# Kernel optimization log

Hardware: AMD Instinct MI355X
Metric: run time of the kernel (lower is better)

## Reference

```python
import jax, jax.numpy as jnp
import numpy as np

B, T, D = 8, 4096, 128
NUM_CB, K = 8, 1024


def setup_inputs() -> dict:
    key = jax.random.key(0)
    k1, k2 = jax.random.split(key)
    embeddings = jax.random.normal(k1, (B, T, D), dtype=jnp.float32)
    # nn.init.uniform_(w, -1/codebook_size, 1/codebook_size)
    codebooks = jax.random.uniform(k2, (NUM_CB, K, D), dtype=jnp.float32,
                                   minval=-1.0 / K, maxval=1.0 / K)
    return {"embeddings": embeddings, "codebooks": codebooks}


def reference(embeddings, codebooks):
    """Residual VQ: returns (codes [B,T,C] int32, quantized [B,T,D], commitment_loss scalar)."""
    Bv, Tv, Dv = embeddings.shape
    flat = embeddings.reshape(-1, Dv)  # [N, D]

    def step(carry, cb_w):  # cb_w: [K, D]
        residual, quant, loss = carry
        # squared euclidean distance; argmin identical to torch.cdist argmin
        d2 = (jnp.sum(residual * residual, axis=-1, keepdims=True)
              - 2.0 * (residual @ cb_w.T)
              + jnp.sum(cb_w * cb_w, axis=-1))  # [N, K]
        idx = jnp.argmin(d2, axis=-1)  # [N]
        ql = cb_w[idx]  # [N, D] gather
        loss = loss + jnp.mean((jax.lax.stop_gradient(residual) - ql) ** 2)
        quant = quant + ql
        residual = residual - jax.lax.stop_gradient(ql)
        return (residual, quant, loss), idx

    init = (flat, jnp.zeros_like(flat), jnp.float32(0.0))
    (_, quant, loss), codes = jax.lax.scan(step, init, codebooks)
    codes = codes.T.reshape(Bv, Tv, codebooks.shape[0])  # [C,N] -> [B,T,C]
    quant = quant.reshape(Bv, Tv, Dv)
    # straight-through estimator
    quantized = embeddings + jax.lax.stop_gradient(quant - embeddings)
    return codes, quantized, loss / codebooks.shape[0]
```

## Files before the change

### kernel.cpp

```cpp
#include <hip/hip_runtime.h>


#define N_ROWS 32768
#define DIM    128
#define KCB    1024
#define NCB    8
#define MB     128
#define PC     256
#define NPASS  (KCB / PC)
#define LDA    132
#define LDB    68

__global__ __launch_bounds__(256) void zero_ws_kernel(double* lws) {
    if (threadIdx.x < NCB) lws[threadIdx.x] = 0.0;
}

__global__ __launch_bounds__(256) void c2_kernel(const float* __restrict__ cbw,
                                                 float* __restrict__ c2g) {
#pragma clang fp contract(off)
    int code = blockIdx.x * 256 + threadIdx.x;
    const float* row = cbw + (size_t)code * DIM;
    float s[8];
    for (int j = 0; j < 8; ++j) { float x = row[j]; s[j] = x * x; }
    for (int m = 1; m < 16; ++m)
        for (int j = 0; j < 8; ++j) { float x = row[m * 8 + j]; float p = x * x; s[j] += p; }
    c2g[code] = ((s[0] + s[1]) + (s[2] + s[3])) + ((s[4] + s[5]) + (s[6] + s[7]));
}

__global__ __launch_bounds__(512, 2) void rvq_kernel(
    const float* __restrict__ emb, const float* __restrict__ cbw,
    const float* __restrict__ c2g, float* __restrict__ out,
    double* __restrict__ lws)
{
    __shared__ float a_lds[MB * LDA];
    __shared__ float b_lds[PC * LDB];
    __shared__ float r2_lds[MB];
    __shared__ float c2_lds[PC];
    __shared__ float scr[4 * MB];
    __shared__ int   codes_lds[NCB * MB];

    const int tid  = threadIdx.x;
    const int tcol = tid & 31;
    const int trow = tid >> 5;
    const size_t base = (size_t)blockIdx.x * MB;

    for (int s = 0; s < 8; ++s) {
        int f4 = s * 512 + tid;
        int r = f4 >> 5, k4 = f4 & 31;
        float4 v = *(const float4*)(emb + (base + r) * DIM + (size_t)k4 * 4);
        *(float4*)(a_lds + r * LDA + k4 * 4) = v;
    }
    __syncthreads();

    {
#pragma clang fp contract(off)
        int r = tid & 127, q = tid >> 7;
        float x0 = a_lds[r * LDA + 2 * q];     float s0 = x0 * x0;
        float x1 = a_lds[r * LDA + 2 * q + 1]; float s1 = x1 * x1;
        for (int m = 1; m < 16; ++m) {
            float y0 = a_lds[r * LDA + m * 8 + 2 * q];     float p0 = y0 * y0; s0 += p0;
            float y1 = a_lds[r * LDA + m * 8 + 2 * q + 1]; float p1 = y1 * y1; s1 += p1;
        }
        scr[q * MB + r] = s0 + s1;
    }
    __syncthreads();
    if (tid < MB) {
#pragma clang fp contract(off)
        float t0 = scr[tid], t1 = scr[MB + tid], t2 = scr[2 * MB + tid], t3 = scr[3 * MB + tid];
        r2_lds[tid] = (t0 + t1) + (t2 + t3);
    }

    const float* ab = a_lds + trow * LDA;
    const float* bb = b_lds + tcol * LDB;

    float minv[8]; int mini[8];

    for (int cb = 0; cb < NCB; ++cb) {
        const float* cbbase = cbw + (size_t)cb * KCB * DIM;
        for (int i = 0; i < 8; ++i) { minv[i] = 3.4e38f; mini[i] = 0; }

        for (int pass = 0; pass < NPASS; ++pass) {
            float acc[8][8];
#pragma unroll
            for (int i = 0; i < 8; ++i)
#pragma unroll
                for (int j = 0; j < 8; ++j) acc[i][j] = 0.f;

            for (int half = 0; half < 2; ++half) {
                __syncthreads();
                const float* bsrc = cbbase + (size_t)pass * PC * DIM + half * 64;
                for (int s = 0; s < 8; ++s) {
                    int f4 = s * 512 + tid;
                    int c = f4 >> 4, k4 = f4 & 15;
                    float4 v = *(const float4*)(bsrc + (size_t)c * DIM + k4 * 4);
                    *(float4*)(b_lds + c * LDB + k4 * 4) = v;
                }
                if (half == 0 && tid < PC) c2_lds[tid] = c2g[cb * KCB + pass * PC + tid];
                __syncthreads();

#pragma unroll
                for (int k4 = 0; k4 < 16; ++k4) {
                    float4 av[8], bv[8];
#pragma unroll
                    for (int i = 0; i < 8; ++i)
                        av[i] = *(const float4*)(ab + i * 16 * LDA + half * 64 + k4 * 4);
#pragma unroll
                    for (int j = 0; j < 8; ++j)
                        bv[j] = *(const float4*)(bb + j * 32 * LDB + k4 * 4);
#pragma unroll
                    for (int i = 0; i < 8; ++i)
#pragma unroll
                        for (int j = 0; j < 8; ++j) {
                            acc[i][j] = fmaf(av[i].x, bv[j].x, acc[i][j]);
                            acc[i][j] = fmaf(av[i].y, bv[j].y, acc[i][j]);
                            acc[i][j] = fmaf(av[i].z, bv[j].z, acc[i][j]);
                            acc[i][j] = fmaf(av[i].w, bv[j].w, acc[i][j]);
                        }
                }
            }

            {
#pragma clang fp contract(off)
                float r2v[8], c2v[8];
                for (int i = 0; i < 8; ++i) r2v[i] = r2_lds[trow + 16 * i];
                for (int j = 0; j < 8; ++j) c2v[j] = c2_lds[tcol + 32 * j];
                for (int i = 0; i < 8; ++i)
                    for (int j = 0; j < 8; ++j) {
                        float t  = r2v[i] - 2.0f * acc[i][j];
                        float d2 = t + c2v[j];
                        int   cg = pass * PC + tcol + 32 * j;
                        if (d2 < minv[i]) { minv[i] = d2; mini[i] = cg; }
                    }
            }
        }

        for (int i = 0; i < 8; ++i) {
            float v = minv[i]; int ix = mini[i];
            for (int m = 1; m <= 16; m <<= 1) {
                float v2 = __shfl_xor(v, m, 64);
                int  ix2 = __shfl_xor(ix, m, 64);
                if (v2 < v || (v2 == v && ix2 < ix)) { v = v2; ix = ix2; }
            }
            if (tcol == 0) codes_lds[cb * MB + (trow + 16 * i)] = ix;
        }
        __syncthreads();

        {
#pragma clang fp contract(off)
            int r = tid & 127, q = tid >> 7;
            int widx = codes_lds[cb * MB + r];
            const float* ql = cbbase + (size_t)widx * DIM;
            float s0 = 0.f, s1 = 0.f;
            double lacc = 0.0;
            for (int m = 0; m < 16; ++m) {
                int k0 = m * 8 + 2 * q;
                float a0 = a_lds[r * LDA + k0];
                float q0 = ql[k0];
                float n0 = a0 - q0;
                a_lds[r * LDA + k0] = n0;
                float p0 = n0 * n0;
                if (m == 0) s0 = p0; else s0 += p0;
                lacc += (double)p0;
                int k1 = k0 + 1;
                float a1 = a_lds[r * LDA + k1];
                float q1 = ql[k1];
                float n1 = a1 - q1;
                a_lds[r * LDA + k1] = n1;
                float p1 = n1 * n1;
                if (m == 0) s1 = p1; else s1 += p1;
                lacc += (double)p1;
            }
            scr[q * MB + r] = s0 + s1;
            for (int off = 32; off > 0; off >>= 1) lacc += __shfl_down(lacc, off, 64);
            if ((tid & 63) == 0) atomicAdd(&lws[cb], lacc);
        }
        __syncthreads();
        if (tid < MB) {
#pragma clang fp contract(off)
            float t0 = scr[tid], t1 = scr[MB + tid], t2 = scr[2 * MB + tid], t3 = scr[3 * MB + tid];
            r2_lds[tid] = (t0 + t1) + (t2 + t3);
        }
    }
    __syncthreads();

    if (tid < MB) {
        int r = tid;
        float4 u, v;
        u.x = (float)codes_lds[0 * MB + r]; u.y = (float)codes_lds[1 * MB + r];
        u.z = (float)codes_lds[2 * MB + r]; u.w = (float)codes_lds[3 * MB + r];
        v.x = (float)codes_lds[4 * MB + r]; v.y = (float)codes_lds[5 * MB + r];
        v.z = (float)codes_lds[6 * MB + r]; v.w = (float)codes_lds[7 * MB + r];
        *(float4*)(out + (base + r) * NCB)     = u;
        *(float4*)(out + (base + r) * NCB + 4) = v;
    }

    {
#pragma clang fp contract(off)
        int r = tid >> 2, q4 = tid & 3;
        size_t rg = base + r;
        int cds[NCB];
        for (int cb = 0; cb < NCB; ++cb) cds[cb] = codes_lds[cb * MB + r];
        float* qout = out + (size_t)N_ROWS * NCB;
        for (int ii = 0; ii < 8; ++ii) {
            int k = q4 * 32 + ii * 4;
            float4 qv = make_float4(0.f, 0.f, 0.f, 0.f);
            for (int cb = 0; cb < NCB; ++cb) {
                float4 cv = *(const float4*)(cbw + ((size_t)cb * KCB + cds[cb]) * DIM + k);
                qv.x += cv.x; qv.y += cv.y; qv.z += cv.z; qv.w += cv.w;
            }
            float4 ev = *(const float4*)(emb + rg * DIM + k);
            float4 ov;
            ov.x = ev.x + (qv.x - ev.x);
            ov.y = ev.y + (qv.y - ev.y);
            ov.z = ev.z + (qv.z - ev.z);
            ov.w = ev.w + (qv.w - ev.w);
            *(float4*)(qout + rg * DIM + k) = ov;
        }
    }
}

__global__ __launch_bounds__(64) void finish_loss_kernel(const double* __restrict__ lws,
                                                         float* __restrict__ out_loss) {
    if (threadIdx.x == 0 && blockIdx.x == 0) {
        float l = 0.f;
        for (int cb = 0; cb < NCB; ++cb) {
            float m = (float)(lws[cb] / 4194304.0);
            l = l + m;
        }
        out_loss[0] = l / 8.0f;
    }
}

extern "C" void kernel_launch(void* const* d_in, const int* in_sizes, int n_in,
                              void* d_out, int out_size, void* d_ws, size_t ws_size,
                              hipStream_t stream) {
    const float* emb = (const float*)d_in[0];
    const float* cbw = (const float*)d_in[1];
    float* out = (float*)d_out;
    double* lws = (double*)d_ws;
    float* c2g = (float*)((char*)d_ws + 256);

    hipLaunchKernelGGL(zero_ws_kernel, dim3(1), dim3(64), 0, stream, lws);
    hipLaunchKernelGGL(c2_kernel, dim3(32), dim3(256), 0, stream, cbw, c2g);
    hipLaunchKernelGGL(rvq_kernel, dim3(256), dim3(512), 0, stream, emb, cbw, c2g, out, lws);
    hipLaunchKernelGGL(finish_loss_kernel, dim3(1), dim3(64), 0, stream, lws,
                       out + (size_t)N_ROWS * NCB + (size_t)N_ROWS * DIM);
}
```

Before: 1.144 ms.

## Remap GEMM thread tile to 16x4 with wave-uniform A rows and swizzled B layout

Changes the per-thread register tile from 8x8 to 16 rows by 4 codes. Each 64-lane wave now shares the same 16 rows, so A reads become LDS broadcasts. The codebook tile is stored k-major as float4 with an XOR swizzle to avoid bank conflicts on B reads, replacing the padded row layout. The argmin reduction now spans the full 64-lane wave. Occupancy is pinned with waves_per_eu. The trade-off is more B loads relative to FMAs per k-step and a different register-pressure profile.

```diff
diff --git a/kernel.cpp b/kernel.cpp
--- a/kernel.cpp
+++ b/kernel.cpp
@@ -8,8 +8,8 @@
 #define MB     128
 #define PC     256
 #define NPASS  (KCB / PC)
+#define KH     64
 #define LDA    132
-#define LDB    68
 
 __global__ __launch_bounds__(256) void zero_ws_kernel(double* lws) {
     if (threadIdx.x < NCB) lws[threadIdx.x] = 0.0;
@@ -27,21 +27,22 @@
     c2g[code] = ((s[0] + s[1]) + (s[2] + s[3])) + ((s[4] + s[5]) + (s[6] + s[7]));
 }
 
-__global__ __launch_bounds__(512, 2) void rvq_kernel(
+__global__ __attribute__((amdgpu_waves_per_eu(2, 2))) __launch_bounds__(512)
+void rvq_kernel(
     const float* __restrict__ emb, const float* __restrict__ cbw,
     const float* __restrict__ c2g, float* __restrict__ out,
     double* __restrict__ lws)
 {
-    __shared__ float a_lds[MB * LDA];
-    __shared__ float b_lds[PC * LDB];
+    __shared__ __align__(16) float a_lds[MB * LDA];
+    __shared__ float4 b_lds4[16 * PC];
     __shared__ float r2_lds[MB];
     __shared__ float c2_lds[PC];
     __shared__ float scr[4 * MB];
     __shared__ int   codes_lds[NCB * MB];
 
     const int tid  = threadIdx.x;
-    const int tcol = tid & 31;
-    const int trow = tid >> 5;
+    const int tcol = tid & 63;
+    const int trow = tid >> 6;
     const size_t base = (size_t)blockIdx.x * MB;
 
     for (int s = 0; s < 8; ++s) {
@@ -70,78 +71,78 @@
         r2_lds[tid] = (t0 + t1) + (t2 + t3);
     }
 
-    const float* ab = a_lds + trow * LDA;
-    const float* bb = b_lds + tcol * LDB;
-
-    float minv[8]; int mini[8];
+    const float* ab = a_lds + trow * 16 * LDA;
+
+    float minv[16]; int mini[16];
 
     for (int cb = 0; cb < NCB; ++cb) {
         const float* cbbase = cbw + (size_t)cb * KCB * DIM;
-        for (int i = 0; i < 8; ++i) { minv[i] = 3.4e38f; mini[i] = 0; }
+        for (int i = 0; i < 16; ++i) { minv[i] = 3.4e38f; mini[i] = 0; }
 
         for (int pass = 0; pass < NPASS; ++pass) {
-            float acc[8][8];
-#pragma unroll
-            for (int i = 0; i < 8; ++i)
-#pragma unroll
-                for (int j = 0; j < 8; ++j) acc[i][j] = 0.f;
+            float acc[16][4];
+#pragma unroll
+            for (int i = 0; i < 16; ++i)
+#pragma unroll
+                for (int j = 0; j < 4; ++j) acc[i][j] = 0.f;
 
             for (int half = 0; half < 2; ++half) {
                 __syncthreads();
-                const float* bsrc = cbbase + (size_t)pass * PC * DIM + half * 64;
+                const float* bsrc = cbbase + (size_t)pass * PC * DIM + half * KH;
                 for (int s = 0; s < 8; ++s) {
                     int f4 = s * 512 + tid;
                     int c = f4 >> 4, k4 = f4 & 15;
                     float4 v = *(const float4*)(bsrc + (size_t)c * DIM + k4 * 4);
-                    *(float4*)(b_lds + c * LDB + k4 * 4) = v;
+                    b_lds4[k4 * 256 + (c ^ (k4 & 7))] = v;
                 }
                 if (half == 0 && tid < PC) c2_lds[tid] = c2g[cb * KCB + pass * PC + tid];
                 __syncthreads();
 
 #pragma unroll
                 for (int k4 = 0; k4 < 16; ++k4) {
-                    float4 av[8], bv[8];
-#pragma unroll
-                    for (int i = 0; i < 8; ++i)
-                        av[i] = *(const float4*)(ab + i * 16 * LDA + half * 64 + k4 * 4);
-#pragma unroll
-                    for (int j = 0; j < 8; ++j)
-                        bv[j] = *(const float4*)(bb + j * 32 * LDB + k4 * 4);
-#pragma unroll
-                    for (int i = 0; i < 8; ++i)
-#pragma unroll
-                        for (int j = 0; j < 8; ++j) {
-                            acc[i][j] = fmaf(av[i].x, bv[j].x, acc[i][j]);
-                            acc[i][j] = fmaf(av[i].y, bv[j].y, acc[i][j]);
-                            acc[i][j] = fmaf(av[i].z, bv[j].z, acc[i][j]);
-                            acc[i][j] = fmaf(av[i].w, bv[j].w, acc[i][j]);
+                    const int bx = tcol ^ (k4 & 7);
+                    float4 bv[4];
+#pragma unroll
+                    for (int j = 0; j < 4; ++j)
+                        bv[j] = b_lds4[k4 * 256 + bx + 64 * j];
+#pragma unroll
+                    for (int i = 0; i < 16; ++i) {
+                        float4 av = *(const float4*)(ab + i * LDA + half * KH + k4 * 4);
+#pragma unroll
+                        for (int j = 0; j < 4; ++j) {
+                            acc[i][j] = fmaf(av.x, bv[j].x, acc[i][j]);
+                            acc[i][j] = fmaf(av.y, bv[j].y, acc[i][j]);
+                            acc[i][j] = fmaf(av.z, bv[j].z, acc[i][j]);
+                            acc[i][j] = fmaf(av.w, bv[j].w, acc[i][j]);
                         }
+                    }
                 }
             }
 
             {
 #pragma clang fp contract(off)
-                float r2v[8], c2v[8];
-                for (int i = 0; i < 8; ++i) r2v[i] = r2_lds[trow + 16 * i];
-                for (int j = 0; j < 8; ++j) c2v[j] = c2_lds[tcol + 32 * j];
-                for (int i = 0; i < 8; ++i)
-                    for (int j = 0; j < 8; ++j) {
-                        float t  = r2v[i] - 2.0f * acc[i][j];
+                float c2v[4];
+                for (int j = 0; j < 4; ++j) c2v[j] = c2_lds[tcol + 64 * j];
+                for (int i = 0; i < 16; ++i) {
+                    float r2v = r2_lds[trow * 16 + i];
+                    for (int j = 0; j < 4; ++j) {
+                        float t  = r2v - 2.0f * acc[i][j];
                         float d2 = t + c2v[j];
-                        int   cg = pass * PC + tcol + 32 * j;
+                        int   cg = pass * PC + tcol + 64 * j;
                         if (d2 < minv[i]) { minv[i] = d2; mini[i] = cg; }
                     }
-            }
-        }
-
-        for (int i = 0; i < 8; ++i) {
+                }
+            }
+        }
+
+        for (int i = 0; i < 16; ++i) {
             float v = minv[i]; int ix = mini[i];
-            for (int m = 1; m <= 16; m <<= 1) {
+            for (int m = 1; m <= 32; m <<= 1) {
                 float v2 = __shfl_xor(v, m, 64);
                 int  ix2 = __shfl_xor(ix, m, 64);
                 if (v2 < v || (v2 == v && ix2 < ix)) { v = v2; ix = ix2; }
             }
-            if (tcol == 0) codes_lds[cb * MB + (trow + 16 * i)] = ix;
+            if (tcol == 0) codes_lds[cb * MB + (trow * 16 + i)] = ix;
         }
         __syncthreads();
 
```

After: 1.142 ms. About the same (-0.2%).
